# Performance work log

Measured on AMD Instinct MI355X. Metric: run time of the kernel, lower is better.

The kernel has to match this reference:

```python
import jax, jax.numpy as jnp
import numpy as np

N = 50000
E = 800000
IN, H, OUT = 128, 96, 64
BN_EPS = 1e-5


def setup_inputs() -> dict:
    key = jax.random.key(0)
    ks = jax.random.split(key, 16)
    x = jax.random.normal(ks[0], (N, IN), dtype=jnp.float32)
    edge_index = jax.random.randint(ks[1], (2, E), 0, N, dtype=jnp.int64)
    edge_weight = jax.random.uniform(ks[2], (E,), dtype=jnp.float32)
    def lin(k, fo, fi):
        # PyG glorot-ish init
        s = 1.0 / np.sqrt(fi)
        return jax.random.uniform(k, (fo, fi), minval=-s, maxval=s, dtype=jnp.float32)
    W1, b1 = lin(ks[3], H, IN), jnp.zeros((H,), jnp.float32)
    W2, b2 = lin(ks[4], H, H), jnp.zeros((H,), jnp.float32)
    W3, b3 = lin(ks[5], OUT, H), jnp.zeros((OUT,), jnp.float32)
    g1 = jnp.ones((H,), jnp.float32); beta1 = jnp.zeros((H,), jnp.float32)
    m1 = 0.1 * jax.random.normal(ks[6], (H,), dtype=jnp.float32)
    v1 = jnp.abs(1.0 + 0.1 * jax.random.normal(ks[7], (H,), dtype=jnp.float32))
    g2 = jnp.ones((H,), jnp.float32); beta2 = jnp.zeros((H,), jnp.float32)
    m2 = 0.1 * jax.random.normal(ks[8], (H,), dtype=jnp.float32)
    v2 = jnp.abs(1.0 + 0.1 * jax.random.normal(ks[9], (H,), dtype=jnp.float32))
    return dict(x=x, edge_index=edge_index, edge_weight=edge_weight,
                W1=W1, b1=b1, W2=W2, b2=b2, W3=W3, b3=b3,
                g1=g1, beta1=beta1, m1=m1, v1=v1,
                g2=g2, beta2=beta2, m2=m2, v2=v2)


def gcn_norm(edge_index, edge_weight, n):
    # PyG gcn_norm with add_self_loops=True, fill_value=1.0
    loop = jnp.arange(n, dtype=edge_index.dtype)
    row = jnp.concatenate([edge_index[0], loop])  # sources
    col = jnp.concatenate([edge_index[1], loop])  # targets
    ew = jnp.concatenate([edge_weight, jnp.ones((n,), edge_weight.dtype)])
    deg = jax.ops.segment_sum(ew, col, num_segments=n)
    dis = jnp.where(deg > 0, jax.lax.rsqrt(deg), 0.0)  # inf -> 0 masked_fill
    norm = dis[row] * ew * dis[col]
    return row, col, norm


def gcn_conv(x, row, col, norm, W, b, n):
    xw = x @ W.T                       # [N, F_out] dense transform first
    msg = norm[:, None] * xw[row]      # [E+N, F_out] gather + edge scale
    out = jax.ops.segment_sum(msg, col, num_segments=n)  # scatter-add
    return out + b


def bn_eval(x, gamma, beta, mean, var):
    return (x - mean) * jax.lax.rsqrt(var + BN_EPS) * gamma + beta


def reference(x, edge_index, edge_weight, W1, b1, W2, b2, W3, b3,
              g1, beta1, m1, v1, g2, beta2, m2, v2):
    n = x.shape[0]
    row, col, norm = gcn_norm(edge_index, edge_weight, n)  # cached=True: shared
    h = gcn_conv(x, row, col, norm, W1, b1, n)
    h = jax.nn.relu(bn_eval(h, g1, beta1, m1, v1))
    h = gcn_conv(h, row, col, norm, W2, b2, n)
    h = jax.nn.relu(bn_eval(h, g2, beta2, m2, v2))
    out = gcn_conv(h, row, col, norm, W3, b3, n)
    return out
```

## Files before the change

### kernel.cpp

```cpp
#include <hip/hip_runtime.h>
#include <hip/hip_fp16.h>


constexpr float BN_EPS = 1e-5f;
constexpr float FIXED_SCALE = 33554432.0f;
constexpr float INV_FIXED_SCALE = 1.0f / 33554432.0f;

typedef _Float16 f16x8 __attribute__((ext_vector_type(8)));
typedef float f32x4 __attribute__((ext_vector_type(4)));


__global__ void k_init(unsigned long long* packed, int n) {
    int i = blockIdx.x * blockDim.x + threadIdx.x;
    if (i < n) packed[i] = 0ull;
}

__global__ void k_deg(const int* __restrict__ col_idx, const float* __restrict__ ew,
                      unsigned long long* packed, int* rank, int e_cnt) {
    int e = blockIdx.x * blockDim.x + threadIdx.x;
    if (e < e_cnt) {
        int c = col_idx[e];
        unsigned int wfix = (unsigned int)(ew[e] * FIXED_SCALE + 0.5f);
        unsigned long long inc = (1ull << 32) | (unsigned long long)wfix;
        unsigned long long old = atomicAdd(&packed[c], inc);
        rank[e] = (int)(old >> 32);
    }
}

__global__ void k_scan1(const unsigned long long* __restrict__ packed,
                        int* bsum, float* dis, int n) {
    __shared__ int s[256];
    int i = blockIdx.x * 256 + threadIdx.x;
    int cnt = 0;
    if (i < n) {
        unsigned long long p = packed[i];
        cnt = (int)(p >> 32);
        float wsum = (float)(unsigned int)(p & 0xffffffffull) * INV_FIXED_SCALE;
        dis[i] = rsqrtf(1.0f + wsum);
    }
    s[threadIdx.x] = cnt;
    __syncthreads();
    for (int off = 128; off > 0; off >>= 1) {
        if (threadIdx.x < off) s[threadIdx.x] += s[threadIdx.x + off];
        __syncthreads();
    }
    if (threadIdx.x == 0) bsum[blockIdx.x] = s[0];
}

__global__ void k_scan2(const int* __restrict__ bsum, int* boff, int nb) {
    __shared__ int s[256];
    int t = threadIdx.x;
    int v = (t < nb) ? bsum[t] : 0;
    s[t] = v;
    __syncthreads();
    for (int off = 1; off < 256; off <<= 1) {
        int x = (t >= off) ? s[t - off] : 0;
        __syncthreads();
        s[t] += x;
        __syncthreads();
    }
    if (t < nb) boff[t] = s[t] - v;
}

__global__ void k_scan3(const unsigned long long* __restrict__ packed,
                        const int* __restrict__ boff,
                        int* row_ptr, int n, int e_total) {
    __shared__ int s[256];
    int t = threadIdx.x;
    int i = blockIdx.x * 256 + t;
    int v = (i < n) ? (int)(packed[i] >> 32) : 0;
    s[t] = v;
    __syncthreads();
    for (int off = 1; off < 256; off <<= 1) {
        int x = (t >= off) ? s[t - off] : 0;
        __syncthreads();
        s[t] += x;
        __syncthreads();
    }
    int ex = s[t] - v + boff[blockIdx.x];
    if (i < n) row_ptr[i] = ex;
    if (i == 0) row_ptr[n] = e_total;
}

__global__ void k_fill(const int* __restrict__ row_idx, const int* __restrict__ col_idx,
                       const float* __restrict__ ew, const float* __restrict__ dis,
                       const int* __restrict__ row_ptr, const int* __restrict__ rank,
                       int2* ep, int e_cnt) {
    int e = blockIdx.x * blockDim.x + threadIdx.x;
    if (e < e_cnt) {
        int r = row_idx[e];
        int c = col_idx[e];
        float nm = dis[r] * ew[e] * dis[c];
        int p = row_ptr[c] + rank[e];
        ep[p] = make_int2(r, __float_as_int(nm));
    }
}


__global__ void k_cvt(const float* __restrict__ src, _Float16* __restrict__ dst,
                      int cnt4) {
    int i = blockIdx.x * blockDim.x + threadIdx.x;
    if (i < cnt4) {
        float4 v = *(const float4*)(src + i * 4);
        __half2 h0 = __floats2half2_rn(v.x, v.y);
        __half2 h1 = __floats2half2_rn(v.z, v.w);
        uint2 u = make_uint2(*(unsigned int*)&h0, *(unsigned int*)&h1);
        *(uint2*)(dst + (size_t)i * 4) = u;
    }
}


template <int K, int F>
__global__ __launch_bounds__(256) void k_gemm_mfma(const _Float16* __restrict__ X,
                                                   const _Float16* __restrict__ Wh,
                                                   _Float16* __restrict__ Y, int n) {
    constexpr int KT = K / 32;
    constexpr int FT = F / 16;
    int wave = threadIdx.x >> 6;
    int lane = threadIdx.x & 63;
    int n0 = (blockIdx.x * 4 + wave) * 16;
    if (n0 >= n) return;
    int quad = lane >> 4;
    int r = lane & 15;

    const f16x8* __restrict__ xrow =
        (const f16x8*)(X + (size_t)(n0 + r) * K + quad * 8);
    f16x8 a[KT];
#pragma unroll
    for (int kt = 0; kt < KT; ++kt) a[kt] = xrow[kt * 4];

    const f16x8* __restrict__ wrow =
        (const f16x8*)(Wh + (size_t)r * K + quad * 8);

    f32x4 acc[FT];
#pragma unroll
    for (int ft = 0; ft < FT; ++ft) acc[ft] = (f32x4){0.f, 0.f, 0.f, 0.f};

#pragma unroll
    for (int kt = 0; kt < KT; ++kt) {
#pragma unroll
        for (int ft = 0; ft < FT; ++ft) {
            f16x8 b = wrow[(size_t)ft * 2 * K + kt * 4];
            acc[ft] = __builtin_amdgcn_mfma_f32_16x16x32_f16(a[kt], b, acc[ft], 0, 0, 0);
        }
    }

#pragma unroll
    for (int ft = 0; ft < FT; ++ft) {
#pragma unroll
        for (int reg = 0; reg < 4; ++reg) {
            int row = n0 + quad * 4 + reg;
            Y[(size_t)row * F + ft * 16 + r] = (_Float16)acc[ft][reg];
        }
    }
}


__device__ inline void h8_acc(uint4 u, float w, float acc[8]) {
    float2 a = __half22float2(*(const __half2*)&u.x);
    float2 b = __half22float2(*(const __half2*)&u.y);
    float2 c = __half22float2(*(const __half2*)&u.z);
    float2 d = __half22float2(*(const __half2*)&u.w);
    acc[0] = fmaf(w, a.x, acc[0]); acc[1] = fmaf(w, a.y, acc[1]);
    acc[2] = fmaf(w, b.x, acc[2]); acc[3] = fmaf(w, b.y, acc[3]);
    acc[4] = fmaf(w, c.x, acc[4]); acc[5] = fmaf(w, c.y, acc[5]);
    acc[6] = fmaf(w, d.x, acc[6]); acc[7] = fmaf(w, d.y, acc[7]);
}

template <int F, bool BN, bool HOUT>
__global__ __launch_bounds__(256) void k_aggr(
    const _Float16* __restrict__ xw, const int* __restrict__ row_ptr,
    const int2* __restrict__ ep,
    const float* __restrict__ dis, const float* __restrict__ bias,
    const float* __restrict__ g, const float* __restrict__ beta,
    const float* __restrict__ m, const float* __restrict__ v,
    void* __restrict__ out, int n) {
    constexpr int FQ = F / 8;
    int tg = blockIdx.x * 256 + threadIdx.x;
    int node = tg / FQ;
    int q = tg - node * FQ;
    if (node >= n) return;

    const uint4* __restrict__ base = (const uint4*)xw;

    float acc[8];
    {
        float d = dis[node];
        float d2 = d * d;
        uint4 sv = base[(size_t)node * FQ + q];
        float2 a = __half22float2(*(const __half2*)&sv.x);
        float2 b = __half22float2(*(const __half2*)&sv.y);
        float2 c = __half22float2(*(const __half2*)&sv.z);
        float2 dd = __half22float2(*(const __half2*)&sv.w);
        acc[0] = d2 * a.x; acc[1] = d2 * a.y;
        acc[2] = d2 * b.x; acc[3] = d2 * b.y;
        acc[4] = d2 * c.x; acc[5] = d2 * c.y;
        acc[6] = d2 * dd.x; acc[7] = d2 * dd.y;
    }

    int e0 = row_ptr[node], e1 = row_ptr[node + 1];
    int e = e0;
    for (; e + 4 <= e1; e += 4) {
        int2 p0 = ep[e + 0];
        int2 p1 = ep[e + 1];
        int2 p2 = ep[e + 2];
        int2 p3 = ep[e + 3];
        uint4 x0 = base[(size_t)p0.x * FQ + q];
        uint4 x1 = base[(size_t)p1.x * FQ + q];
        uint4 x2 = base[(size_t)p2.x * FQ + q];
        uint4 x3 = base[(size_t)p3.x * FQ + q];
        h8_acc(x0, __int_as_float(p0.y), acc);
        h8_acc(x1, __int_as_float(p1.y), acc);
        h8_acc(x2, __int_as_float(p2.y), acc);
        h8_acc(x3, __int_as_float(p3.y), acc);
    }
    for (; e < e1; ++e) {
        int2 p = ep[e];
        uint4 xv = base[(size_t)p.x * FQ + q];
        h8_acc(xv, __int_as_float(p.y), acc);
    }

    int fb = q * 8;
    const float4* bb = (const float4*)(bias + fb);
    float4 b0 = bb[0], b1 = bb[1];
    acc[0] += b0.x; acc[1] += b0.y; acc[2] += b0.z; acc[3] += b0.w;
    acc[4] += b1.x; acc[5] += b1.y; acc[6] += b1.z; acc[7] += b1.w;
    if (BN) {
        const float* gp = g + fb;
        const float* bp = beta + fb;
        const float* mp = m + fb;
        const float* vp = v + fb;
#pragma unroll
        for (int j = 0; j < 8; ++j) {
            acc[j] = fmaxf((acc[j] - mp[j]) * rsqrtf(vp[j] + BN_EPS) * gp[j] + bp[j], 0.f);
        }
    }
    if (HOUT) {
        __half2 h0 = __floats2half2_rn(acc[0], acc[1]);
        __half2 h1 = __floats2half2_rn(acc[2], acc[3]);
        __half2 h2 = __floats2half2_rn(acc[4], acc[5]);
        __half2 h3 = __floats2half2_rn(acc[6], acc[7]);
        uint4 u = make_uint4(*(unsigned int*)&h0, *(unsigned int*)&h1,
                             *(unsigned int*)&h2, *(unsigned int*)&h3);
        ((uint4*)out)[(size_t)node * FQ + q] = u;
    } else {
        float4* op = (float4*)((float*)out + (size_t)node * F + fb);
        op[0] = make_float4(acc[0], acc[1], acc[2], acc[3]);
        op[1] = make_float4(acc[4], acc[5], acc[6], acc[7]);
    }
}


extern "C" void kernel_launch(void* const* d_in, const int* in_sizes, int n_in,
                              void* d_out, int out_size, void* d_ws, size_t ws_size,
                              hipStream_t stream) {
    constexpr int IN = 128, H = 96, OUT = 64;

    const float* x   = (const float*)d_in[0];
    const int*   ei  = (const int*)d_in[1];
    const float* ew  = (const float*)d_in[2];
    const float* W1  = (const float*)d_in[3];
    const float* b1  = (const float*)d_in[4];
    const float* W2  = (const float*)d_in[5];
    const float* b2  = (const float*)d_in[6];
    const float* W3  = (const float*)d_in[7];
    const float* b3  = (const float*)d_in[8];
    const float* g1  = (const float*)d_in[9];
    const float* be1 = (const float*)d_in[10];
    const float* m1  = (const float*)d_in[11];
    const float* v1  = (const float*)d_in[12];
    const float* g2  = (const float*)d_in[13];
    const float* be2 = (const float*)d_in[14];
    const float* m2  = (const float*)d_in[15];
    const float* v2  = (const float*)d_in[16];

    const int N = in_sizes[0] / IN;
    const int E = in_sizes[2];
    const int* row_idx = ei;
    const int* col_idx = ei + E;

    char* ws = (char*)d_ws;
    size_t off = 0;
    auto alloc = [&](size_t bytes) -> void* {
        void* p = ws + off;
        off = (off + bytes + 255) & ~(size_t)255;
        return p;
    };
    unsigned long long* packed = (unsigned long long*)alloc((size_t)N * 8);
    float*     dis     = (float*)alloc((size_t)N * 4);
    int*       row_ptr = (int*)alloc((size_t)(N + 1) * 4);
    int*       bsum    = (int*)alloc(256 * 4);
    int*       boff    = (int*)alloc(256 * 4);
    int*       rank    = (int*)alloc((size_t)E * 4);
    int2*      ep      = (int2*)alloc((size_t)E * 8);
    _Float16*  xh      = (_Float16*)alloc((size_t)N * IN * 2);
    _Float16*  w1h     = (_Float16*)alloc((size_t)H * IN * 2);
    _Float16*  w2h     = (_Float16*)alloc((size_t)H * H * 2);
    _Float16*  w3h     = (_Float16*)alloc((size_t)OUT * H * 2);
    _Float16*  bufA    = (_Float16*)alloc((size_t)N * H * 2);
    _Float16*  bufB    = (_Float16*)alloc((size_t)N * H * 2);
    (void)ws_size; (void)n_in; (void)out_size;

    const int NB = (N + 255) / 256;

    k_init<<<NB, 256, 0, stream>>>(packed, N);
    k_deg<<<(E + 255) / 256, 256, 0, stream>>>(col_idx, ew, packed, rank, E);
    k_scan1<<<NB, 256, 0, stream>>>(packed, bsum, dis, N);
    k_scan2<<<1, 256, 0, stream>>>(bsum, boff, NB);
    k_scan3<<<NB, 256, 0, stream>>>(packed, boff, row_ptr, N, E);
    k_fill<<<(E + 255) / 256, 256, 0, stream>>>(row_idx, col_idx, ew, dis,
                                                row_ptr, rank, ep, E);

    k_cvt<<<(N * IN / 4 + 255) / 256, 256, 0, stream>>>(x, xh, N * IN / 4);
    k_cvt<<<(H * IN / 4 + 255) / 256, 256, 0, stream>>>(W1, w1h, H * IN / 4);
    k_cvt<<<(H * H / 4 + 255) / 256, 256, 0, stream>>>(W2, w2h, H * H / 4);
    k_cvt<<<(OUT * H / 4 + 255) / 256, 256, 0, stream>>>(W3, w3h, OUT * H / 4);

    const int GG = (N / 16 + 3) / 4;
    const int GA96 = ((size_t)N * (H / 8) + 255) / 256;
    const int GA64 = ((size_t)N * (OUT / 8) + 255) / 256;

    k_gemm_mfma<IN, H><<<GG, 256, 0, stream>>>(xh, w1h, bufA, N);
    k_aggr<H, true, true><<<GA96, 256, 0, stream>>>(
        bufA, row_ptr, ep, dis, b1, g1, be1, m1, v1, bufB, N);

    k_gemm_mfma<H, H><<<GG, 256, 0, stream>>>(bufB, w2h, bufA, N);
    k_aggr<H, true, true><<<GA96, 256, 0, stream>>>(
        bufA, row_ptr, ep, dis, b2, g2, be2, m2, v2, bufB, N);

    k_gemm_mfma<H, OUT><<<GG, 256, 0, stream>>>(bufB, w3h, bufA, N);
    k_aggr<OUT, false, false><<<GA64, 256, 0, stream>>>(
        bufA, row_ptr, ep, dis, b3, nullptr, nullptr, nullptr, nullptr,
        d_out, N);
}
```

Measured before the change: 286.1 us.

## Slice features into per-block column strips, compress edge entries, fuse conversions

The GEMM output is stored as 8 feature slices of 12 (or 8) columns, each laid out contiguously per node. Aggregation blocks then handle one slice per thread-node, which keeps each slice's gathered working set small enough to stay cache resident. Edge entries are packed into 32 bits as a 16-bit source index and a 16-bit fixed-point norm, halving edge traffic. The x-to-fp16 conversion is folded into the first GEMM, the weight conversions are merged into the degree kernel, and the init kernel is replaced by a memset. The 16-bit node index only works while N stays below 65536, and quantising the norm reduces accuracy.

```diff
diff --git a/kernel.cpp b/kernel.cpp
--- a/kernel.cpp
+++ b/kernel.cpp
@@ -5,25 +5,41 @@
 constexpr float BN_EPS = 1e-5f;
 constexpr float FIXED_SCALE = 33554432.0f;
 constexpr float INV_FIXED_SCALE = 1.0f / 33554432.0f;
+constexpr float NORM_SCALE = 32768.0f;
+constexpr float INV_NORM_SCALE = 1.0f / 32768.0f;
 
 typedef _Float16 f16x8 __attribute__((ext_vector_type(8)));
 typedef float f32x4 __attribute__((ext_vector_type(4)));
 
 
-__global__ void k_init(unsigned long long* packed, int n) {
-    int i = blockIdx.x * blockDim.x + threadIdx.x;
-    if (i < n) packed[i] = 0ull;
-}
-
-__global__ void k_deg(const int* __restrict__ col_idx, const float* __restrict__ ew,
-                      unsigned long long* packed, int* rank, int e_cnt) {
-    int e = blockIdx.x * blockDim.x + threadIdx.x;
-    if (e < e_cnt) {
-        int c = col_idx[e];
-        unsigned int wfix = (unsigned int)(ew[e] * FIXED_SCALE + 0.5f);
-        unsigned long long inc = (1ull << 32) | (unsigned long long)wfix;
-        unsigned long long old = atomicAdd(&packed[c], inc);
-        rank[e] = (int)(old >> 32);
+__global__ void k_deg_cvt(const int* __restrict__ col_idx, const float* __restrict__ ew,
+                          unsigned long long* packed, int* rank, int e_cnt, int deg_b,
+                          const float* __restrict__ W1, const float* __restrict__ W2,
+                          const float* __restrict__ W3, _Float16* __restrict__ wh,
+                          int w1n4, int w2n4, int w3n4) {
+    if (blockIdx.x < deg_b) {
+        int e = blockIdx.x * 256 + threadIdx.x;
+        if (e < e_cnt) {
+            int c = col_idx[e];
+            unsigned int wfix = (unsigned int)(ew[e] * FIXED_SCALE + 0.5f);
+            unsigned long long inc = (1ull << 32) | (unsigned long long)wfix;
+            unsigned long long old = atomicAdd(&packed[c], inc);
+            rank[e] = (int)(old >> 32);
+        }
+    } else {
+        int i = (blockIdx.x - deg_b) * 256 + threadIdx.x;
+        int total = w1n4 + w2n4 + w3n4;
+        if (i < total) {
+            const float* src; int off;
+            if (i < w1n4) { src = W1; off = i; }
+            else if (i < w1n4 + w2n4) { src = W2; off = i - w1n4; }
+            else { src = W3; off = i - w1n4 - w2n4; }
+            float4 v = ((const float4*)src)[off];
+            __half2 h0 = __floats2half2_rn(v.x, v.y);
+            __half2 h1 = __floats2half2_rn(v.z, v.w);
+            uint2 u = make_uint2(*(unsigned int*)&h0, *(unsigned int*)&h1);
+            *(uint2*)(wh + (size_t)i * 4) = u;
+        }
     }
 }
 
@@ -85,37 +101,27 @@
 __global__ void k_fill(const int* __restrict__ row_idx, const int* __restrict__ col_idx,
                        const float* __restrict__ ew, const float* __restrict__ dis,
                        const int* __restrict__ row_ptr, const int* __restrict__ rank,
-                       int2* ep, int e_cnt) {
-    int e = blockIdx.x * blockDim.x + threadIdx.x;
+                       unsigned* ep, int e_cnt) {
+    int e = blockIdx.x * 256 + threadIdx.x;
     if (e < e_cnt) {
         int r = row_idx[e];
         int c = col_idx[e];
         float nm = dis[r] * ew[e] * dis[c];
+        unsigned q = (unsigned)(nm * NORM_SCALE + 0.5f);
+        if (q > 65535u) q = 65535u;
         int p = row_ptr[c] + rank[e];
-        ep[p] = make_int2(r, __float_as_int(nm));
-    }
-}
-
-
-__global__ void k_cvt(const float* __restrict__ src, _Float16* __restrict__ dst,
-                      int cnt4) {
-    int i = blockIdx.x * blockDim.x + threadIdx.x;
-    if (i < cnt4) {
-        float4 v = *(const float4*)(src + i * 4);
-        __half2 h0 = __floats2half2_rn(v.x, v.y);
-        __half2 h1 = __floats2half2_rn(v.z, v.w);
-        uint2 u = make_uint2(*(unsigned int*)&h0, *(unsigned int*)&h1);
-        *(uint2*)(dst + (size_t)i * 4) = u;
-    }
-}
-
-
-template <int K, int F>
-__global__ __launch_bounds__(256) void k_gemm_mfma(const _Float16* __restrict__ X,
-                                                   const _Float16* __restrict__ Wh,
-                                                   _Float16* __restrict__ Y, int n) {
+        ep[p] = ((unsigned)r << 16) | q;
+    }
+}
+
+
+template <int K, int F, int SHW, bool F32IN>
+__global__ __launch_bounds__(256) void k_gemm(const void* __restrict__ Xin,
+                                              const _Float16* __restrict__ Wh,
+                                              _Float16* __restrict__ Ys, int n) {
     constexpr int KT = K / 32;
     constexpr int FT = F / 16;
+    constexpr int SROW = (SHW == 12) ? 16 : 8;
     int wave = threadIdx.x >> 6;
     int lane = threadIdx.x & 63;
     int n0 = (blockIdx.x * 4 + wave) * 16;
@@ -123,14 +129,24 @@
     int quad = lane >> 4;
     int r = lane & 15;
 
-    const f16x8* __restrict__ xrow =
-        (const f16x8*)(X + (size_t)(n0 + r) * K + quad * 8);
     f16x8 a[KT];
-#pragma unroll
-    for (int kt = 0; kt < KT; ++kt) a[kt] = xrow[kt * 4];
-
-    const f16x8* __restrict__ wrow =
-        (const f16x8*)(Wh + (size_t)r * K + quad * 8);
+    if (F32IN) {
+        const float* xr = (const float*)Xin + (size_t)(n0 + r) * K + quad * 8;
+#pragma unroll
+        for (int kt = 0; kt < KT; ++kt) {
+            float4 v0 = *(const float4*)(xr + kt * 32);
+            float4 v1 = *(const float4*)(xr + kt * 32 + 4);
+            f16x8 t = {(_Float16)v0.x, (_Float16)v0.y, (_Float16)v0.z, (_Float16)v0.w,
+                       (_Float16)v1.x, (_Float16)v1.y, (_Float16)v1.z, (_Float16)v1.w};
+            a[kt] = t;
+        }
+    } else {
+        const f16x8* xr = (const f16x8*)((const _Float16*)Xin + (size_t)(n0 + r) * K + quad * 8);
+#pragma unroll
+        for (int kt = 0; kt < KT; ++kt) a[kt] = xr[kt * 4];
+    }
+
+    const f16x8* __restrict__ wrow = (const f16x8*)(Wh + (size_t)r * K + quad * 8);
 
     f32x4 acc[FT];
 #pragma unroll
@@ -147,106 +163,139 @@
 
 #pragma unroll
     for (int ft = 0; ft < FT; ++ft) {
+        int f = ft * 16 + r;
+        int s_, off;
+        if (SHW == 12) { s_ = f / 12; off = f - s_ * 12; }
+        else           { s_ = f >> 3; off = f & 7; }
+        _Float16* dst = Ys + (size_t)s_ * n * SROW + off;
 #pragma unroll
         for (int reg = 0; reg < 4; ++reg) {
             int row = n0 + quad * 4 + reg;
-            Y[(size_t)row * F + ft * 16 + r] = (_Float16)acc[ft][reg];
-        }
-    }
-}
-
-
-__device__ inline void h8_acc(uint4 u, float w, float acc[8]) {
-    float2 a = __half22float2(*(const __half2*)&u.x);
-    float2 b = __half22float2(*(const __half2*)&u.y);
-    float2 c = __half22float2(*(const __half2*)&u.z);
-    float2 d = __half22float2(*(const __half2*)&u.w);
-    acc[0] = fmaf(w, a.x, acc[0]); acc[1] = fmaf(w, a.y, acc[1]);
-    acc[2] = fmaf(w, b.x, acc[2]); acc[3] = fmaf(w, b.y, acc[3]);
-    acc[4] = fmaf(w, c.x, acc[4]); acc[5] = fmaf(w, c.y, acc[5]);
-    acc[6] = fmaf(w, d.x, acc[6]); acc[7] = fmaf(w, d.y, acc[7]);
-}
-
-template <int F, bool BN, bool HOUT>
+            dst[(size_t)row * SROW] = (_Float16)acc[ft][reg];
+        }
+    }
+}
+
+
+__device__ inline void cvt8(uint4 u, float* f) {
+    float2 t;
+    t = __half22float2(*(const __half2*)&u.x); f[0] = t.x; f[1] = t.y;
+    t = __half22float2(*(const __half2*)&u.y); f[2] = t.x; f[3] = t.y;
+    t = __half22float2(*(const __half2*)&u.z); f[4] = t.x; f[5] = t.y;
+    t = __half22float2(*(const __half2*)&u.w); f[6] = t.x; f[7] = t.y;
+}
+
+__device__ inline void fma8(uint4 u, float w, float* acc) {
+    float2 t;
+    t = __half22float2(*(const __half2*)&u.x); acc[0] = fmaf(w, t.x, acc[0]); acc[1] = fmaf(w, t.y, acc[1]);
+    t = __half22float2(*(const __half2*)&u.y); acc[2] = fmaf(w, t.x, acc[2]); acc[3] = fmaf(w, t.y, acc[3]);
+    t = __half22float2(*(const __half2*)&u.z); acc[4] = fmaf(w, t.x, acc[4]); acc[5] = fmaf(w, t.y, acc[5]);
+    t = __half22float2(*(const __half2*)&u.w); acc[6] = fmaf(w, t.x, acc[6]); acc[7] = fmaf(w, t.y, acc[7]);
+}
+
+__device__ inline void fma4(uint4 u, float w, float* acc) {
+    float2 t;
+    t = __half22float2(*(const __half2*)&u.x); acc[0] = fmaf(w, t.x, acc[0]); acc[1] = fmaf(w, t.y, acc[1]);
+    t = __half22float2(*(const __half2*)&u.y); acc[2] = fmaf(w, t.x, acc[2]); acc[3] = fmaf(w, t.y, acc[3]);
+}
+
+template <int F, int SHW, bool BN, bool F32OUT>
 __global__ __launch_bounds__(256) void k_aggr(
-    const _Float16* __restrict__ xw, const int* __restrict__ row_ptr,
-    const int2* __restrict__ ep,
-    const float* __restrict__ dis, const float* __restrict__ bias,
-    const float* __restrict__ g, const float* __restrict__ beta,
-    const float* __restrict__ m, const float* __restrict__ v,
-    void* __restrict__ out, int n) {
-    constexpr int FQ = F / 8;
-    int tg = blockIdx.x * 256 + threadIdx.x;
-    int node = tg / FQ;
-    int q = tg - node * FQ;
+    const _Float16* __restrict__ Xs, const int* __restrict__ row_ptr,
+    const unsigned* __restrict__ ep, const float* __restrict__ dis,
+    const float* __restrict__ bias, const float* __restrict__ g,
+    const float* __restrict__ beta, const float* __restrict__ m,
+    const float* __restrict__ v, void* __restrict__ out, int n) {
+    constexpr int SROW = (SHW == 12) ? 16 : 8;
+    int s = blockIdx.x & 7;
+    int node = (blockIdx.x >> 3) * 256 + threadIdx.x;
     if (node >= n) return;
-
-    const uint4* __restrict__ base = (const uint4*)xw;
-
-    float acc[8];
+    const _Float16* __restrict__ base = Xs + (size_t)s * n * SROW;
+
+    float acc[SHW];
     {
         float d = dis[node];
         float d2 = d * d;
-        uint4 sv = base[(size_t)node * FQ + q];
-        float2 a = __half22float2(*(const __half2*)&sv.x);
-        float2 b = __half22float2(*(const __half2*)&sv.y);
-        float2 c = __half22float2(*(const __half2*)&sv.z);
-        float2 dd = __half22float2(*(const __half2*)&sv.w);
-        acc[0] = d2 * a.x; acc[1] = d2 * a.y;
-        acc[2] = d2 * b.x; acc[3] = d2 * b.y;
-        acc[4] = d2 * c.x; acc[5] = d2 * c.y;
-        acc[6] = d2 * dd.x; acc[7] = d2 * dd.y;
+        const _Float16* sp = base + (size_t)node * SROW;
+        float t[SHW];
+        uint4 u0 = *(const uint4*)sp;
+        cvt8(u0, t);
+        if (SHW == 12) {
+            uint4 u1 = *(const uint4*)(sp + 8);
+            float2 w0 = __half22float2(*(const __half2*)&u1.x);
+            float2 w1 = __half22float2(*(const __half2*)&u1.y);
+            t[8] = w0.x; t[9] = w0.y; t[10] = w1.x; t[11] = w1.y;
+        }
+#pragma unroll
+        for (int j = 0; j < SHW; ++j) acc[j] = d2 * t[j];
     }
 
     int e0 = row_ptr[node], e1 = row_ptr[node + 1];
     int e = e0;
     for (; e + 4 <= e1; e += 4) {
-        int2 p0 = ep[e + 0];
-        int2 p1 = ep[e + 1];
-        int2 p2 = ep[e + 2];
-        int2 p3 = ep[e + 3];
-        uint4 x0 = base[(size_t)p0.x * FQ + q];
-        uint4 x1 = base[(size_t)p1.x * FQ + q];
-        uint4 x2 = base[(size_t)p2.x * FQ + q];
-        uint4 x3 = base[(size_t)p3.x * FQ + q];
-        h8_acc(x0, __int_as_float(p0.y), acc);
-        h8_acc(x1, __int_as_float(p1.y), acc);
-        h8_acc(x2, __int_as_float(p2.y), acc);
-        h8_acc(x3, __int_as_float(p3.y), acc);
+        unsigned p0 = ep[e + 0], p1 = ep[e + 1], p2 = ep[e + 2], p3 = ep[e + 3];
+        const _Float16* r0 = base + (size_t)(p0 >> 16) * SROW;
+        const _Float16* r1 = base + (size_t)(p1 >> 16) * SROW;
+        const _Float16* r2 = base + (size_t)(p2 >> 16) * SROW;
+        const _Float16* r3 = base + (size_t)(p3 >> 16) * SROW;
+        uint4 a0 = *(const uint4*)r0;
+        uint4 a1 = *(const uint4*)r1;
+        uint4 a2 = *(const uint4*)r2;
+        uint4 a3 = *(const uint4*)r3;
+        float w0 = (float)(p0 & 0xffffu) * INV_NORM_SCALE;
+        float w1 = (float)(p1 & 0xffffu) * INV_NORM_SCALE;
+        float w2 = (float)(p2 & 0xffffu) * INV_NORM_SCALE;
+        float w3 = (float)(p3 & 0xffffu) * INV_NORM_SCALE;
+        fma8(a0, w0, acc); fma8(a1, w1, acc); fma8(a2, w2, acc); fma8(a3, w3, acc);
+        if (SHW == 12) {
+            uint4 b0 = *(const uint4*)(r0 + 8);
+            uint4 b1 = *(const uint4*)(r1 + 8);
+            uint4 b2 = *(const uint4*)(r2 + 8);
+            uint4 b3 = *(const uint4*)(r3 + 8);
+            fma4(b0, w0, acc + 8); fma4(b1, w1, acc + 8);
+            fma4(b2, w2, acc + 8); fma4(b3, w3, acc + 8);
+        }
     }
     for (; e < e1; ++e) {
-        int2 p = ep[e];
-        uint4 xv = base[(size_t)p.x * FQ + q];
-        h8_acc(xv, __int_as_float(p.y), acc);
-    }
-
-    int fb = q * 8;
-    const float4* bb = (const float4*)(bias + fb);
-    float4 b0 = bb[0], b1 = bb[1];
-    acc[0] += b0.x; acc[1] += b0.y; acc[2] += b0.z; acc[3] += b0.w;
-    acc[4] += b1.x; acc[5] += b1.y; acc[6] += b1.z; acc[7] += b1.w;
+        unsigned p = ep[e];
+        const _Float16* r0 = base + (size_t)(p >> 16) * SROW;
+        float w = (float)(p & 0xffffu) * INV_NORM_SCALE;
+        uint4 a0 = *(const uint4*)r0;
+        fma8(a0, w, acc);
+        if (SHW == 12) {
+            uint4 b0 = *(const uint4*)(r0 + 8);
+            fma4(b0, w, acc + 8);
+        }
+    }
+
+    int fb = s * SHW;
+#pragma unroll
+    for (int j = 0; j < SHW; ++j) acc[j] += bias[fb + j];
     if (BN) {
-        const float* gp = g + fb;
-        const float* bp = beta + fb;
-        const float* mp = m + fb;
-        const float* vp = v + fb;
-#pragma unroll
-        for (int j = 0; j < 8; ++j) {
-            acc[j] = fmaxf((acc[j] - mp[j]) * rsqrtf(vp[j] + BN_EPS) * gp[j] + bp[j], 0.f);
-        }
-    }
-    if (HOUT) {
+#pragma unroll
+        for (int j = 0; j < SHW; ++j) {
+            acc[j] = fmaxf((acc[j] - m[fb + j]) * rsqrtf(v[fb + j] + BN_EPS) * g[fb + j]
+                           + beta[fb + j], 0.f);
+        }
+    }
+
+    if (F32OUT) {
+        float* op = (float*)out + (size_t)node * F + fb;
+        *(float4*)(op + 0) = make_float4(acc[0], acc[1], acc[2], acc[3]);
+        *(float4*)(op + 4) = make_float4(acc[4], acc[5], acc[6], acc[7]);
+    } else {
+        _Float16* op = (_Float16*)out + (size_t)node * F + fb;
         __half2 h0 = __floats2half2_rn(acc[0], acc[1]);
         __half2 h1 = __floats2half2_rn(acc[2], acc[3]);
         __half2 h2 = __floats2half2_rn(acc[4], acc[5]);
         __half2 h3 = __floats2half2_rn(acc[6], acc[7]);
-        uint4 u = make_uint4(*(unsigned int*)&h0, *(unsigned int*)&h1,
-                             *(unsigned int*)&h2, *(unsigned int*)&h3);
-        ((uint4*)out)[(size_t)node * FQ + q] = u;
-    } else {
-        float4* op = (float4*)((float*)out + (size_t)node * F + fb);
-        op[0] = make_float4(acc[0], acc[1], acc[2], acc[3]);
-        op[1] = make_float4(acc[4], acc[5], acc[6], acc[7]);
+        *(uint2*)(op + 0) = make_uint2(*(unsigned*)&h0, *(unsigned*)&h1);
+        *(uint2*)(op + 4) = make_uint2(*(unsigned*)&h2, *(unsigned*)&h3);
+        if (SHW == 12) {
+            __half2 h4 = __floats2half2_rn(acc[8], acc[9]);
+            __half2 h5 = __floats2half2_rn(acc[10], acc[11]);
+            *(uint2*)(op + 8) = make_uint2(*(unsigned*)&h4, *(unsigned*)&h5);
+        }
     }
 }
 
@@ -292,44 +341,41 @@
     int*       bsum    = (int*)alloc(256 * 4);
     int*       boff    = (int*)alloc(256 * 4);
     int*       rank    = (int*)alloc((size_t)E * 4);
-    int2*      ep      = (int2*)alloc((size_t)E * 8);
-    _Float16*  xh      = (_Float16*)alloc((size_t)N * IN * 2);
-    _Float16*  w1h     = (_Float16*)alloc((size_t)H * IN * 2);
-    _Float16*  w2h     = (_Float16*)alloc((size_t)H * H * 2);
-    _Float16*  w3h     = (_Float16*)alloc((size_t)OUT * H * 2);
-    _Float16*  bufA    = (_Float16*)alloc((size_t)N * H * 2);
-    _Float16*  bufB    = (_Float16*)alloc((size_t)N * H * 2);
+    unsigned*  ep      = (unsigned*)alloc((size_t)E * 4);
+    _Float16*  wh      = (_Float16*)alloc((size_t)(H * IN + H * H + OUT * H) * 2);
+    _Float16*  xws     = (_Float16*)alloc((size_t)8 * N * 16 * 2);
+    _Float16*  rowbuf  = (_Float16*)alloc((size_t)N * H * 2);
     (void)ws_size; (void)n_in; (void)out_size;
 
+    _Float16* w1h = wh;
+    _Float16* w2h = wh + (size_t)H * IN;
+    _Float16* w3h = wh + (size_t)H * IN + (size_t)H * H;
+    constexpr int W1N4 = H * IN / 4, W2N4 = H * H / 4, W3N4 = OUT * H / 4;
+
     const int NB = (N + 255) / 256;
-
-    k_init<<<NB, 256, 0, stream>>>(packed, N);
-    k_deg<<<(E + 255) / 256, 256, 0, stream>>>(col_idx, ew, packed, rank, E);
+    const int DEG_B = (E + 255) / 256;
+    const int CVT_B = (W1N4 + W2N4 + W3N4 + 255) / 256;
+
+    hipMemsetAsync(packed, 0, (size_t)N * 8, stream);
+    k_deg_cvt<<<DEG_B + CVT_B, 256, 0, stream>>>(col_idx, ew, packed, rank, E, DEG_B,
+                                                 W1, W2, W3, wh, W1N4, W2N4, W3N4);
     k_scan1<<<NB, 256, 0, stream>>>(packed, bsum, dis, N);
     k_scan2<<<1, 256, 0, stream>>>(bsum, boff, NB);
     k_scan3<<<NB, 256, 0, stream>>>(packed, boff, row_ptr, N, E);
-    k_fill<<<(E + 255) / 256, 256, 0, stream>>>(row_idx, col_idx, ew, dis,
-                                                row_ptr, rank, ep, E);
-
-    k_cvt<<<(N * IN / 4 + 255) / 256, 256, 0, stream>>>(x, xh, N * IN / 4);
-    k_cvt<<<(H * IN / 4 + 255) / 256, 256, 0, stream>>>(W1, w1h, H * IN / 4);
-    k_cvt<<<(H * H / 4 + 255) / 256, 256, 0, stream>>>(W2, w2h, H * H / 4);
-    k_cvt<<<(OUT * H / 4 + 255) / 256, 256, 0, stream>>>(W3, w3h, OUT * H / 4);
+    k_fill<<<DEG_B, 256, 0, stream>>>(row_idx, col_idx, ew, dis, row_ptr, rank, ep, E);
 
     const int GG = (N / 16 + 3) / 4;
-    const int GA96 = ((size_t)N * (H / 8) + 255) / 256;
-    const int GA64 = ((size_t)N * (OUT / 8) + 255) / 256;
-
-    k_gemm_mfma<IN, H><<<GG, 256, 0, stream>>>(xh, w1h, bufA, N);
-    k_aggr<H, true, true><<<GA96, 256, 0, stream>>>(
-        bufA, row_ptr, ep, dis, b1, g1, be1, m1, v1, bufB, N);
-
-    k_gemm_mfma<H, H><<<GG, 256, 0, stream>>>(bufB, w2h, bufA, N);
-    k_aggr<H, true, true><<<GA96, 256, 0, stream>>>(
-        bufA, row_ptr, ep, dis, b2, g2, be2, m2, v2, bufB, N);
-
-    k_gemm_mfma<H, OUT><<<GG, 256, 0, stream>>>(bufB, w3h, bufA, N);
-    k_aggr<OUT, false, false><<<GA64, 256, 0, stream>>>(
-        bufA, row_ptr, ep, dis, b3, nullptr, nullptr, nullptr, nullptr,
-        d_out, N);
-}
+    const int GA = 8 * NB;
+
+    k_gemm<IN, H, 12, true><<<GG, 256, 0, stream>>>(x, w1h, xws, N);
+    k_aggr<H, 12, true, false><<<GA, 256, 0, stream>>>(
+        xws, row_ptr, ep, dis, b1, g1, be1, m1, v1, rowbuf, N);
+
+    k_gemm<H, H, 12, false><<<GG, 256, 0, stream>>>(rowbuf, w2h, xws, N);
+    k_aggr<H, 12, true, false><<<GA, 256, 0, stream>>>(
+        xws, row_ptr, ep, dis, b2, g2, be2, m2, v2, rowbuf, N);
+
+    k_gemm<H, OUT, 8, false><<<GG, 256, 0, stream>>>(rowbuf, w3h, xws, N);
+    k_aggr<OUT, 8, false, true><<<GA, 256, 0, stream>>>(
+        xws, row_ptr, ep, dis, b3, nullptr, nullptr, nullptr, nullptr, d_out, N);
+}
```

Result: slower. 391.7 us (+36.9%).

## Fuse preprocessing kernels, pack edge entries to 32 bits, convert x inside GEMM

Applied to the files above, without the earlier changes.

Merges the degree atomics, the first GEMM (now reading fp32 x and W1 and converting in registers) and the W2/W3 conversions into one multi-role launch. It also folds the two scan passes into one and replaces k_init with a memset. Edge entries shrink from 8 to 4 bytes by packing a 16-bit source index with a 16-bit fixed-point norm, halving edge-stream traffic in each aggregation. This cuts launches and removes the x fp16 copy pass. The 16-bit source index cannot represent N=50000 above 65535, and the 16-bit quantized norm saturates and loses precision, so accuracy is at risk.

```diff
diff --git a/kernel.cpp b/kernel.cpp
--- a/kernel.cpp
+++ b/kernel.cpp
@@ -5,27 +5,120 @@
 constexpr float BN_EPS = 1e-5f;
 constexpr float FIXED_SCALE = 33554432.0f;
 constexpr float INV_FIXED_SCALE = 1.0f / 33554432.0f;
+constexpr float NORM_SCALE = 32768.0f;
+constexpr float INV_NORM_SCALE = 1.0f / 32768.0f;
 
 typedef _Float16 f16x8 __attribute__((ext_vector_type(8)));
 typedef float f32x4 __attribute__((ext_vector_type(4)));
 
 
-__global__ void k_init(unsigned long long* packed, int n) {
-    int i = blockIdx.x * blockDim.x + threadIdx.x;
-    if (i < n) packed[i] = 0ull;
-}
-
-__global__ void k_deg(const int* __restrict__ col_idx, const float* __restrict__ ew,
-                      unsigned long long* packed, int* rank, int e_cnt) {
-    int e = blockIdx.x * blockDim.x + threadIdx.x;
-    if (e < e_cnt) {
-        int c = col_idx[e];
-        unsigned int wfix = (unsigned int)(ew[e] * FIXED_SCALE + 0.5f);
-        unsigned long long inc = (1ull << 32) | (unsigned long long)wfix;
-        unsigned long long old = atomicAdd(&packed[c], inc);
-        rank[e] = (int)(old >> 32);
-    }
-}
+template <int K, int F, bool F32X, bool F32W>
+__device__ __forceinline__ void gemm_body(const void* __restrict__ Xin,
+                                          const void* __restrict__ Win,
+                                          _Float16* __restrict__ Y, int n,
+                                          int bid, int tid) {
+    constexpr int KT = K / 32;
+    constexpr int FT = F / 16;
+    int wave = tid >> 6;
+    int lane = tid & 63;
+    int n0 = (bid * 4 + wave) * 16;
+    if (n0 >= n) return;
+    int quad = lane >> 4;
+    int r = lane & 15;
+
+    f16x8 a[KT];
+    if (F32X) {
+        const float* xr = (const float*)Xin + (size_t)(n0 + r) * K + quad * 8;
+#pragma unroll
+        for (int kt = 0; kt < KT; ++kt) {
+            float4 v0 = *(const float4*)(xr + kt * 32);
+            float4 v1 = *(const float4*)(xr + kt * 32 + 4);
+            f16x8 t = {(_Float16)v0.x, (_Float16)v0.y, (_Float16)v0.z, (_Float16)v0.w,
+                       (_Float16)v1.x, (_Float16)v1.y, (_Float16)v1.z, (_Float16)v1.w};
+            a[kt] = t;
+        }
+    } else {
+        const f16x8* xr = (const f16x8*)((const _Float16*)Xin + (size_t)(n0 + r) * K + quad * 8);
+#pragma unroll
+        for (int kt = 0; kt < KT; ++kt) a[kt] = xr[kt * 4];
+    }
+
+    f32x4 acc[FT];
+#pragma unroll
+    for (int ft = 0; ft < FT; ++ft) acc[ft] = (f32x4){0.f, 0.f, 0.f, 0.f};
+
+#pragma unroll
+    for (int kt = 0; kt < KT; ++kt) {
+#pragma unroll
+        for (int ft = 0; ft < FT; ++ft) {
+            f16x8 b;
+            if (F32W) {
+                const float* wr = (const float*)Win + (size_t)(ft * 16 + r) * K + kt * 32 + quad * 8;
+                float4 v0 = *(const float4*)wr;
+                float4 v1 = *(const float4*)(wr + 4);
+                f16x8 t = {(_Float16)v0.x, (_Float16)v0.y, (_Float16)v0.z, (_Float16)v0.w,
+                           (_Float16)v1.x, (_Float16)v1.y, (_Float16)v1.z, (_Float16)v1.w};
+                b = t;
+            } else {
+                b = *(const f16x8*)((const _Float16*)Win + (size_t)(ft * 16 + r) * K + kt * 32 + quad * 8);
+            }
+            acc[ft] = __builtin_amdgcn_mfma_f32_16x16x32_f16(a[kt], b, acc[ft], 0, 0, 0);
+        }
+    }
+
+#pragma unroll
+    for (int ft = 0; ft < FT; ++ft) {
+#pragma unroll
+        for (int reg = 0; reg < 4; ++reg) {
+            int row = n0 + quad * 4 + reg;
+            Y[(size_t)row * F + ft * 16 + r] = (_Float16)acc[ft][reg];
+        }
+    }
+}
+
+template <int K, int F>
+__global__ __launch_bounds__(256) void k_gemm(const _Float16* __restrict__ X,
+                                              const _Float16* __restrict__ Wh,
+                                              _Float16* __restrict__ Y, int n) {
+    gemm_body<K, F, false, false>(X, Wh, Y, n, blockIdx.x, threadIdx.x);
+}
+
+
+__global__ __launch_bounds__(256) void k_mega(
+    const int* __restrict__ col_idx, const float* __restrict__ ew,
+    unsigned long long* packed, int* rank, int e_cnt, int deg_b,
+    const float* __restrict__ x, const float* __restrict__ W1,
+    _Float16* __restrict__ bufA, int n, int gg,
+    const float* __restrict__ W2, const float* __restrict__ W3,
+    _Float16* __restrict__ w2h, _Float16* __restrict__ w3h,
+    int w2n4, int w3n4) {
+    int b = blockIdx.x;
+    if (b < deg_b) {
+        int e = b * 256 + threadIdx.x;
+        if (e < e_cnt) {
+            int c = col_idx[e];
+            unsigned int wfix = (unsigned int)(ew[e] * FIXED_SCALE + 0.5f);
+            unsigned long long inc = (1ull << 32) | (unsigned long long)wfix;
+            unsigned long long old = atomicAdd(&packed[c], inc);
+            rank[e] = (int)(old >> 32);
+        }
+    } else if (b < deg_b + gg) {
+        gemm_body<128, 96, true, true>(x, W1, bufA, n, b - deg_b, threadIdx.x);
+    } else {
+        int i = (b - deg_b - gg) * 256 + threadIdx.x;
+        const float* src;
+        _Float16* dst;
+        int off;
+        if (i < w2n4) { src = W2; dst = w2h; off = i; }
+        else if (i < w2n4 + w3n4) { src = W3; dst = w3h; off = i - w2n4; }
+        else return;
+        float4 v = ((const float4*)src)[off];
+        __half2 h0 = __floats2half2_rn(v.x, v.y);
+        __half2 h1 = __floats2half2_rn(v.z, v.w);
+        *(uint2*)(dst + (size_t)off * 4) = make_uint2(*(unsigned*)&h0, *(unsigned*)&h1);
+    }
+}
+
 
 __global__ void k_scan1(const unsigned long long* __restrict__ packed,
                         int* bsum, float* dis, int n) {
@@ -47,26 +140,23 @@
     if (threadIdx.x == 0) bsum[blockIdx.x] = s[0];
 }
 
-__global__ void k_scan2(const int* __restrict__ bsum, int* boff, int nb) {
+__global__ void k_scan23(const unsigned long long* __restrict__ packed,
+                         const int* __restrict__ bsum,
+                         int* row_ptr, int n, int e_total, int nb) {
+    __shared__ int sb[256];
     __shared__ int s[256];
     int t = threadIdx.x;
-    int v = (t < nb) ? bsum[t] : 0;
-    s[t] = v;
+    int bv = (t < nb) ? bsum[t] : 0;
+    sb[t] = bv;
     __syncthreads();
     for (int off = 1; off < 256; off <<= 1) {
-        int x = (t >= off) ? s[t - off] : 0;
-        __syncthreads();
-        s[t] += x;
-        __syncthreads();
-    }
-    if (t < nb) boff[t] = s[t] - v;
-}
-
-__global__ void k_scan3(const unsigned long long* __restrict__ packed,
-                        const int* __restrict__ boff,
-                        int* row_ptr, int n, int e_total) {
-    __shared__ int s[256];
-    int t = threadIdx.x;
+        int x = (t >= off) ? sb[t - off] : 0;
+        __syncthreads();
+        sb[t] += x;
+        __syncthreads();
+    }
+    int boff = (blockIdx.x == 0) ? 0 : sb[blockIdx.x - 1];
+
     int i = blockIdx.x * 256 + t;
     int v = (i < n) ? (int)(packed[i] >> 32) : 0;
     s[t] = v;
@@ -77,7 +167,7 @@
         s[t] += x;
         __syncthreads();
     }
-    int ex = s[t] - v + boff[blockIdx.x];
+    int ex = s[t] - v + boff;
     if (i < n) row_ptr[i] = ex;
     if (i == 0) row_ptr[n] = e_total;
 }
@@ -85,73 +175,16 @@
 __global__ void k_fill(const int* __restrict__ row_idx, const int* __restrict__ col_idx,
                        const float* __restrict__ ew, const float* __restrict__ dis,
                        const int* __restrict__ row_ptr, const int* __restrict__ rank,
-                       int2* ep, int e_cnt) {
-    int e = blockIdx.x * blockDim.x + threadIdx.x;
+                       unsigned* ep, int e_cnt) {
+    int e = blockIdx.x * 256 + threadIdx.x;
     if (e < e_cnt) {
         int r = row_idx[e];
         int c = col_idx[e];
         float nm = dis[r] * ew[e] * dis[c];
+        unsigned q = (unsigned)(nm * NORM_SCALE + 0.5f);
+        if (q > 65535u) q = 65535u;
         int p = row_ptr[c] + rank[e];
-        ep[p] = make_int2(r, __float_as_int(nm));
-    }
-}
-
-
-__global__ void k_cvt(const float* __restrict__ src, _Float16* __restrict__ dst,
-                      int cnt4) {
-    int i = blockIdx.x * blockDim.x + threadIdx.x;
-    if (i < cnt4) {
-        float4 v = *(const float4*)(src + i * 4);
-        __half2 h0 = __floats2half2_rn(v.x, v.y);
-        __half2 h1 = __floats2half2_rn(v.z, v.w);
-        uint2 u = make_uint2(*(unsigned int*)&h0, *(unsigned int*)&h1);
-        *(uint2*)(dst + (size_t)i * 4) = u;
-    }
-}
-
-
-template <int K, int F>
-__global__ __launch_bounds__(256) void k_gemm_mfma(const _Float16* __restrict__ X,
-                                                   const _Float16* __restrict__ Wh,
-                                                   _Float16* __restrict__ Y, int n) {
-    constexpr int KT = K / 32;
-    constexpr int FT = F / 16;
-    int wave = threadIdx.x >> 6;
-    int lane = threadIdx.x & 63;
-    int n0 = (blockIdx.x * 4 + wave) * 16;
-    if (n0 >= n) return;
-    int quad = lane >> 4;
-    int r = lane & 15;
-
-    const f16x8* __restrict__ xrow =
-        (const f16x8*)(X + (size_t)(n0 + r) * K + quad * 8);
-    f16x8 a[KT];
-#pragma unroll
-    for (int kt = 0; kt < KT; ++kt) a[kt] = xrow[kt * 4];
-
-    const f16x8* __restrict__ wrow =
-        (const f16x8*)(Wh + (size_t)r * K + quad * 8);
-
-    f32x4 acc[FT];
-#pragma unroll
-    for (int ft = 0; ft < FT; ++ft) acc[ft] = (f32x4){0.f, 0.f, 0.f, 0.f};
-
-#pragma unroll
-    for (int kt = 0; kt < KT; ++kt) {
-#pragma unroll
-        for (int ft = 0; ft < FT; ++ft) {
-            f16x8 b = wrow[(size_t)ft * 2 * K + kt * 4];
-            acc[ft] = __builtin_amdgcn_mfma_f32_16x16x32_f16(a[kt], b, acc[ft], 0, 0, 0);
-        }
-    }
-
-#pragma unroll
-    for (int ft = 0; ft < FT; ++ft) {
-#pragma unroll
-        for (int reg = 0; reg < 4; ++reg) {
-            int row = n0 + quad * 4 + reg;
-            Y[(size_t)row * F + ft * 16 + r] = (_Float16)acc[ft][reg];
-        }
+        ep[p] = ((unsigned)r << 16) | q;
     }
 }
 
@@ -167,10 +200,10 @@
     acc[6] = fmaf(w, d.x, acc[6]); acc[7] = fmaf(w, d.y, acc[7]);
 }
 
-template <int F, bool BN, bool HOUT>
+template <int F, bool BN, bool F32OUT>
 __global__ __launch_bounds__(256) void k_aggr(
     const _Float16* __restrict__ xw, const int* __restrict__ row_ptr,
-    const int2* __restrict__ ep,
+    const unsigned* __restrict__ ep,
     const float* __restrict__ dis, const float* __restrict__ bias,
     const float* __restrict__ g, const float* __restrict__ beta,
     const float* __restrict__ m, const float* __restrict__ v,
@@ -188,36 +221,29 @@
         float d = dis[node];
         float d2 = d * d;
         uint4 sv = base[(size_t)node * FQ + q];
-        float2 a = __half22float2(*(const __half2*)&sv.x);
-        float2 b = __half22float2(*(const __half2*)&sv.y);
-        float2 c = __half22float2(*(const __half2*)&sv.z);
-        float2 dd = __half22float2(*(const __half2*)&sv.w);
-        acc[0] = d2 * a.x; acc[1] = d2 * a.y;
-        acc[2] = d2 * b.x; acc[3] = d2 * b.y;
-        acc[4] = d2 * c.x; acc[5] = d2 * c.y;
-        acc[6] = d2 * dd.x; acc[7] = d2 * dd.y;
+        float t[8];
+        h8_acc(sv, d2, (float*)memset(t, 0, sizeof(t)));
+#pragma unroll
+        for (int j = 0; j < 8; ++j) acc[j] = t[j];
     }
 
     int e0 = row_ptr[node], e1 = row_ptr[node + 1];
     int e = e0;
     for (; e + 4 <= e1; e += 4) {
-        int2 p0 = ep[e + 0];
-        int2 p1 = ep[e + 1];
-        int2 p2 = ep[e + 2];
-        int2 p3 = ep[e + 3];
-        uint4 x0 = base[(size_t)p0.x * FQ + q];
-        uint4 x1 = base[(size_t)p1.x * FQ + q];
-        uint4 x2 = base[(size_t)p2.x * FQ + q];
-        uint4 x3 = base[(size_t)p3.x * FQ + q];
-        h8_acc(x0, __int_as_float(p0.y), acc);
-        h8_acc(x1, __int_as_float(p1.y), acc);
-        h8_acc(x2, __int_as_float(p2.y), acc);
-        h8_acc(x3, __int_as_float(p3.y), acc);
+        unsigned p0 = ep[e + 0], p1 = ep[e + 1], p2 = ep[e + 2], p3 = ep[e + 3];
+        uint4 x0 = base[(size_t)(p0 >> 16) * FQ + q];
+        uint4 x1 = base[(size_t)(p1 >> 16) * FQ + q];
+        uint4 x2 = base[(size_t)(p2 >> 16) * FQ + q];
+        uint4 x3 = base[(size_t)(p3 >> 16) * FQ + q];
+        h8_acc(x0, (float)(p0 & 0xffffu) * INV_NORM_SCALE, acc);
+        h8_acc(x1, (float)(p1 & 0xffffu) * INV_NORM_SCALE, acc);
+        h8_acc(x2, (float)(p2 & 0xffffu) * INV_NORM_SCALE, acc);
+        h8_acc(x3, (float)(p3 & 0xffffu) * INV_NORM_SCALE, acc);
     }
     for (; e < e1; ++e) {
-        int2 p = ep[e];
-        uint4 xv = base[(size_t)p.x * FQ + q];
-        h8_acc(xv, __int_as_float(p.y), acc);
+        unsigned p = ep[e];
+        uint4 xv = base[(size_t)(p >> 16) * FQ + q];
+        h8_acc(xv, (float)(p & 0xffffu) * INV_NORM_SCALE, acc);
     }
 
     int fb = q * 8;
@@ -235,18 +261,18 @@
             acc[j] = fmaxf((acc[j] - mp[j]) * rsqrtf(vp[j] + BN_EPS) * gp[j] + bp[j], 0.f);
         }
     }
-    if (HOUT) {
+    if (F32OUT) {
+        float* op = (float*)out + (size_t)node * F + fb;
+        *(float4*)(op + 0) = make_float4(acc[0], acc[1], acc[2], acc[3]);
+        *(float4*)(op + 4) = make_float4(acc[4], acc[5], acc[6], acc[7]);
+    } else {
         __half2 h0 = __floats2half2_rn(acc[0], acc[1]);
         __half2 h1 = __floats2half2_rn(acc[2], acc[3]);
         __half2 h2 = __floats2half2_rn(acc[4], acc[5]);
         __half2 h3 = __floats2half2_rn(acc[6], acc[7]);
-        uint4 u = make_uint4(*(unsigned int*)&h0, *(unsigned int*)&h1,
-                             *(unsigned int*)&h2, *(unsigned int*)&h3);
+        uint4 u = make_uint4(*(unsigned*)&h0, *(unsigned*)&h1,
+                             *(unsigned*)&h2, *(unsigned*)&h3);
         ((uint4*)out)[(size_t)node * FQ + q] = u;
-    } else {
-        float4* op = (float4*)((float*)out + (size_t)node * F + fb);
-        op[0] = make_float4(acc[0], acc[1], acc[2], acc[3]);
-        op[1] = make_float4(acc[4], acc[5], acc[6], acc[7]);
     }
 }
 
@@ -290,46 +316,39 @@
     float*     dis     = (float*)alloc((size_t)N * 4);
     int*       row_ptr = (int*)alloc((size_t)(N + 1) * 4);
     int*       bsum    = (int*)alloc(256 * 4);
-    int*       boff    = (int*)alloc(256 * 4);
     int*       rank    = (int*)alloc((size_t)E * 4);
-    int2*      ep      = (int2*)alloc((size_t)E * 8);
-    _Float16*  xh      = (_Float16*)alloc((size_t)N * IN * 2);
-    _Float16*  w1h     = (_Float16*)alloc((size_t)H * IN * 2);
+    unsigned*  ep      = (unsigned*)alloc((size_t)E * 4);
     _Float16*  w2h     = (_Float16*)alloc((size_t)H * H * 2);
     _Float16*  w3h     = (_Float16*)alloc((size_t)OUT * H * 2);
     _Float16*  bufA    = (_Float16*)alloc((size_t)N * H * 2);
     _Float16*  bufB    = (_Float16*)alloc((size_t)N * H * 2);
     (void)ws_size; (void)n_in; (void)out_size;
 
+    constexpr int W2N4 = H * H / 4, W3N4 = OUT * H / 4;
     const int NB = (N + 255) / 256;
-
-    k_init<<<NB, 256, 0, stream>>>(packed, N);
-    k_deg<<<(E + 255) / 256, 256, 0, stream>>>(col_idx, ew, packed, rank, E);
+    const int DEG_B = (E + 255) / 256;
+    const int GG = (N / 16 + 3) / 4;
+    const int CVT_B = (W2N4 + W3N4 + 255) / 256;
+
+    hipMemsetAsync(packed, 0, (size_t)N * 8, stream);
+    k_mega<<<DEG_B + GG + CVT_B, 256, 0, stream>>>(
+        col_idx, ew, packed, rank, E, DEG_B,
+        x, W1, bufA, N, GG, W2, W3, w2h, w3h, W2N4, W3N4);
     k_scan1<<<NB, 256, 0, stream>>>(packed, bsum, dis, N);
-    k_scan2<<<1, 256, 0, stream>>>(bsum, boff, NB);
-    k_scan3<<<NB, 256, 0, stream>>>(packed, boff, row_ptr, N, E);
-    k_fill<<<(E + 255) / 256, 256, 0, stream>>>(row_idx, col_idx, ew, dis,
-                                                row_ptr, rank, ep, E);
-
-    k_cvt<<<(N * IN / 4 + 255) / 256, 256, 0, stream>>>(x, xh, N * IN / 4);
-    k_cvt<<<(H * IN / 4 + 255) / 256, 256, 0, stream>>>(W1, w1h, H * IN / 4);
-    k_cvt<<<(H * H / 4 + 255) / 256, 256, 0, stream>>>(W2, w2h, H * H / 4);
-    k_cvt<<<(OUT * H / 4 + 255) / 256, 256, 0, stream>>>(W3, w3h, OUT * H / 4);
-
-    const int GG = (N / 16 + 3) / 4;
+    k_scan23<<<NB, 256, 0, stream>>>(packed, bsum, row_ptr, N, E, NB);
+    k_fill<<<DEG_B, 256, 0, stream>>>(row_idx, col_idx, ew, dis, row_ptr, rank, ep, E);
+
     const int GA96 = ((size_t)N * (H / 8) + 255) / 256;
     const int GA64 = ((size_t)N * (OUT / 8) + 255) / 256;
 
-    k_gemm_mfma<IN, H><<<GG, 256, 0, stream>>>(xh, w1h, bufA, N);
-    k_aggr<H, true, true><<<GA96, 256, 0, stream>>>(
+    k_aggr<H, true, false><<<GA96, 256, 0, stream>>>(
         bufA, row_ptr, ep, dis, b1, g1, be1, m1, v1, bufB, N);
 
-    k_gemm_mfma<H, H><<<GG, 256, 0, stream>>>(bufB, w2h, bufA, N);
-    k_aggr<H, true, true><<<GA96, 256, 0, stream>>>(
+    k_gemm<H, H><<<GG, 256, 0, stream>>>(bufB, w2h, bufA, N);
+    k_aggr<H, true, false><<<GA96, 256, 0, stream>>>(
         bufA, row_ptr, ep, dis, b2, g2, be2, m2, v2, bufB, N);
 
-    k_gemm_mfma<H, OUT><<<GG, 256, 0, stream>>>(bufB, w3h, bufA, N);
-    k_aggr<OUT, false, false><<<GA64, 256, 0, stream>>>(
-        bufA, row_ptr, ep, dis, b3, nullptr, nullptr, nullptr, nullptr,
-        d_out, N);
-}
+    k_gemm<H, OUT><<<GG, 256, 0, stream>>>(bufB, w3h, bufA, N);
+    k_aggr<OUT, false, true><<<GA64, 256, 0, stream>>>(
+        bufA, row_ptr, ep, dis, b3, nullptr, nullptr, nullptr, nullptr, d_out, N);
+}
```

Result: no change. 281.4 us (-1.7%).
